# Optimization experiments

Measured on AMD Instinct MI355X. Metric: run time of the kernel, lower is better.

## Reference

```python
import jax, jax.numpy as jnp
import numpy as np

B, T, C, H = 8, 2048, 1024, 128  # batch, seq, embed_dim, head_size

def setup_inputs() -> dict:
    key = jax.random.key(0)
    kx, kk, kq, kv = jax.random.split(key, 4)
    s = 1.0 / np.sqrt(C)  # ~nn.Linear init scale
    return {
        "x": jax.random.normal(kx, (B, T, C), dtype=jnp.float32),
        "Wk": jax.random.normal(kk, (H, C), dtype=jnp.float32) * s,
        "Wq": jax.random.normal(kq, (H, C), dtype=jnp.float32) * s,
        "Wv": jax.random.normal(kv, (H, C), dtype=jnp.float32) * s,
    }

def reference(x, Wk, Wq, Wv):
    b, t, c = x.shape
    # Faithful to source: q uses the KEY projection (bug in original); Wq is unused.
    k = jnp.einsum('btc,hc->bth', x, Wk)   # [B,T,H]
    q = jnp.einsum('btc,hc->bth', x, Wk)   # [B,T,H]  (self.key used for q)
    v = jnp.einsum('btc,hc->bth', x, Wv)   # [B,T,H]
    score = jnp.einsum('bqh,bkh->bqk', q, k) * (c ** -0.5)  # scale by C, per source
    causal = jnp.tril(jnp.ones((t, t), dtype=bool))
    score = jnp.where(causal, score, -jnp.inf)
    attn = jax.nn.softmax(score, axis=-1)   # [B,T,T]
    out = jnp.einsum('bqk,bkh->bqh', attn, v)  # [B,T,H]
    return out
```

## Files before the change

kernel.cpp:

```cpp
#include <hip/hip_runtime.h>
#include <hip/hip_bf16.h>

#define BATCH 8
#define SEQ   2048
#define EMB   1024
#define HD    128

typedef __attribute__((ext_vector_type(8))) short bf16x8;
typedef __attribute__((ext_vector_type(4))) float f32x4;

__device__ __forceinline__ short f2bf(float f) {
    union { float f; unsigned u; } v; v.f = f;
    unsigned r = v.u + 0x7fffu + ((v.u >> 16) & 1u);
    return (short)(r >> 16);
}

__device__ __forceinline__ void glds16(const short* g, short* l) {
    __builtin_amdgcn_global_load_lds(
        (const __attribute__((address_space(1))) unsigned int*)g,
        (__attribute__((address_space(3))) unsigned int*)l, 16, 0, 0);
}


__global__ void prep_w(const float* __restrict__ Wk, const float* __restrict__ Wv,
                       short* __restrict__ Wimg) {
    int g  = blockIdx.x * 256 + threadIdx.x;
    int q  = g & 3;
    int l  = (g >> 2) & 15;
    int f  = (g >> 6) & 7;
    int kk = (g >> 9) & 1;
    int kc = (g >> 10) & 15;
    int nh = (g >> 14) & 1;
    const float* src = (nh ? Wv : Wk) + (size_t)(f * 16 + l) * EMB + kc * 64 + kk * 32 + q * 8;
    float4 f0 = *(const float4*)src;
    float4 f1 = *(const float4*)(src + 4);
    bf16x8 v;
    v[0]=f2bf(f0.x); v[1]=f2bf(f0.y); v[2]=f2bf(f0.z); v[3]=f2bf(f0.w);
    v[4]=f2bf(f1.x); v[5]=f2bf(f1.y); v[6]=f2bf(f1.z); v[7]=f2bf(f1.w);
    *(bf16x8*)&Wimg[(size_t)g * 8] = v;
}

__global__ __launch_bounds__(512, 2)
void proj_kernel(const float* __restrict__ x, const short* __restrict__ Wimg,
                 short* __restrict__ Kimg,
                 short* __restrict__ Vimg)
{
    __shared__ __align__(16) union {
        short A[2][64][72];
        short ep[16384];
    } sm;

    const int tid  = threadIdx.x;
    const int wave = tid >> 6;
    const int lane = tid & 63;
    const int quad = lane >> 4;
    const int l16  = lane & 15;
    const int nh   = wave >> 2;
    const int fb   = (wave & 3) * 2;
    const int mt   = blockIdx.x;
    const int row0 = mt * 64;

    const int srow = tid >> 3, sseg = tid & 7;
    const float* xsrc = x + (size_t)(row0 + srow) * EMB + sseg * 8;
    const short* wsrc = Wimg + (size_t)nh * 131072;

    f32x4 acc[4][2];
#pragma unroll
    for (int a = 0; a < 4; ++a)
#pragma unroll
        for (int c = 0; c < 2; ++c) acc[a][c] = f32x4{0.f, 0.f, 0.f, 0.f};

    {
        float4 a0 = *(const float4*)xsrc;
        float4 a1 = *(const float4*)(xsrc + 4);
        bf16x8 v;
        v[0]=f2bf(a0.x); v[1]=f2bf(a0.y); v[2]=f2bf(a0.z); v[3]=f2bf(a0.w);
        v[4]=f2bf(a1.x); v[5]=f2bf(a1.y); v[6]=f2bf(a1.z); v[7]=f2bf(a1.w);
        *(bf16x8*)&sm.A[0][srow][sseg * 8] = v;
    }
    __syncthreads();

    for (int kc = 0; kc < 16; ++kc) {
        const int cur = kc & 1;
        float4 a0, a1;
        if (kc < 15) {
            const float* nx = xsrc + (kc + 1) * 64;
            a0 = *(const float4*)nx;
            a1 = *(const float4*)(nx + 4);
        }
        const short* wc = wsrc + (size_t)kc * 8192;
        bf16x8 bfr[2][2];
#pragma unroll
        for (int kk = 0; kk < 2; ++kk)
#pragma unroll
            for (int f2 = 0; f2 < 2; ++f2)
                bfr[kk][f2] = *(const bf16x8*)&wc[(((kk * 8 + fb + f2) * 16 + l16) * 4 + quad) * 8];

#pragma unroll
        for (int kk = 0; kk < 2; ++kk)
#pragma unroll
            for (int mf = 0; mf < 4; ++mf) {
                bf16x8 af = *(const bf16x8*)&sm.A[cur][mf * 16 + l16][kk * 32 + quad * 8];
#pragma unroll
                for (int f2 = 0; f2 < 2; ++f2)
                    acc[mf][f2] = __builtin_amdgcn_mfma_f32_16x16x32_bf16(af, bfr[kk][f2], acc[mf][f2], 0, 0, 0);
            }

        if (kc < 15) {
            bf16x8 v;
            v[0]=f2bf(a0.x); v[1]=f2bf(a0.y); v[2]=f2bf(a0.z); v[3]=f2bf(a0.w);
            v[4]=f2bf(a1.x); v[5]=f2bf(a1.y); v[6]=f2bf(a1.z); v[7]=f2bf(a1.w);
            *(bf16x8*)&sm.A[cur ^ 1][srow][sseg * 8] = v;
        }
        __syncthreads();
    }

#pragma unroll
    for (int mf = 0; mf < 4; ++mf)
#pragma unroll
        for (int f2 = 0; f2 < 2; ++f2)
#pragma unroll
            for (int r = 0; r < 4; ++r) {
                const int row = mf * 16 + quad * 4 + r;
                const int h   = (fb + f2) * 16 + l16;
                int idx;
                if (nh == 0)
                    idx = ((((h >> 5) * 4 + (row >> 4)) * 16 + (row & 15)) * 4 + ((h >> 3) & 3)) * 8 + (h & 7);
                else
                    idx = 8192 + ((((row >> 5) * 8 + (h >> 4)) * 16 + (h & 15)) * 4 + ((row >> 3) & 3)) * 8 + (row & 7);
                sm.ep[idx] = f2bf(acc[mf][f2][r]);
            }
    __syncthreads();

    {
#pragma unroll
        for (int i = 0; i < 4; ++i) {
            const int g = i * 512 + tid;
            short* dst = (g < 1024) ? (Kimg + (size_t)mt * 8192 + g * 8)
                                    : (Vimg + (size_t)mt * 8192 + (g - 1024) * 8);
            *(bf16x8*)dst = *(const bf16x8*)&sm.ep[g * 8];
        }
    }
}

#define LOG2E 1.4426950408889634f

__global__ __launch_bounds__(256, 2)
void attn_kernel(const short* __restrict__ Kimg,
                 const short* __restrict__ Vimg,
                 float* __restrict__ out)
{
    __shared__ __align__(16) short kbuf[2][8192];
    __shared__ __align__(16) short vbuf[8192];
    __shared__ __align__(16) short ps[2][1024];
    __shared__ float lsum[4][16];

    const int tid  = threadIdx.x;
    const int wave = tid >> 6;
    const int lane = tid & 63;
    const int quad = lane >> 4;
    const int l16  = lane & 15;

    const int b    = blockIdx.x & 7;
    const int gg   = blockIdx.x >> 3;
    const int G    = (blockIdx.x < 256) ? (63 - gg) : (gg - 32);
    const int qsel = wave >> 1;
    const int p    = wave & 1;
    const int qt   = 2 * G + qsel;
    const int n    = (G >> 1) + 1;

    const short* Kb = Kimg + (size_t)b * 32 * 8192;
    const short* Vb = Vimg + (size_t)b * 32 * 8192;

    bf16x8 qf[4];
    {
        const short* qi = Kb + (size_t)(qt >> 2) * 8192;
        const int jsq = qt & 3;
#pragma unroll
        for (int kc = 0; kc < 4; ++kc)
            qf[kc] = *(const bf16x8*)&qi[(((kc * 4 + jsq) * 16 + l16) * 4 + quad) * 8];
    }

    f32x4 O[4];
#pragma unroll
    for (int f = 0; f < 4; ++f) O[f] = f32x4{0.f, 0.f, 0.f, 0.f};
    float lp[4] = {0.f, 0.f, 0.f, 0.f};

    const float coef = LOG2E * 0.03125f;
    short* psq = ps[qsel];

    {
        const short* sk = Kb + wave * 2048 + lane * 8;
#pragma unroll
        for (int i = 0; i < 4; ++i)
            glds16(sk + i * 512, &kbuf[0][wave * 2048 + i * 512]);
    }

    int cur = 0;
    for (int jt = 0; jt < n; ++jt) {
        asm volatile("s_waitcnt vmcnt(0)" ::: "memory");
        __builtin_amdgcn_s_barrier();

        {
            const short* sv = Vb + (size_t)jt * 8192 + wave * 2048 + lane * 8;
#pragma unroll
            for (int i = 0; i < 4; ++i)
                glds16(sv + i * 512, &vbuf[wave * 2048 + i * 512]);
        }
        const bool more = (jt + 1 < n);
        if (more) {
            const short* sk = Kb + (size_t)(jt + 1) * 8192 + wave * 2048 + lane * 8;
#pragma unroll
            for (int i = 0; i < 4; ++i)
                glds16(sk + i * 512, &kbuf[cur ^ 1][wave * 2048 + i * 512]);
        }

        const short* kt = kbuf[cur];
        f32x4 S[2];
        S[0] = f32x4{0.f, 0.f, 0.f, 0.f};
        S[1] = f32x4{0.f, 0.f, 0.f, 0.f};
#pragma unroll
        for (int kc = 0; kc < 4; ++kc)
#pragma unroll
            for (int j2 = 0; j2 < 2; ++j2) {
                bf16x8 kf = *(const bf16x8*)&kt[((kc * 4 + p * 2 + j2) * 64 + l16 * 4 + quad) * 8];
                S[j2] = __builtin_amdgcn_mfma_f32_16x16x32_bf16(qf[kc], kf, S[j2], 0, 0, 0);
            }

        const bool diag = (jt == n - 1);
#pragma unroll
        for (int j2 = 0; j2 < 2; ++j2) {
            const int js = p * 2 + j2;
            const int jj = jt * 64 + js * 16 + l16;
            const int cb = js * 2 + (l16 >> 3);
            const int e  = l16 & 7;
#pragma unroll
            for (int r = 0; r < 4; ++r) {
                float vv = S[j2][r] * coef;
                if (diag && (jj > qt * 16 + quad * 4 + r)) vv = -INFINITY;
                float pe = exp2f(vv);
                lp[r] += pe;
                const int i8 = quad * 4 + r;
                psq[(i8 * 8 + (cb ^ (i8 & 7))) * 8 + e] = f2bf(pe);
            }
        }

        if (more) asm volatile("s_waitcnt vmcnt(4) lgkmcnt(0)" ::: "memory");
        else      asm volatile("s_waitcnt vmcnt(0) lgkmcnt(0)" ::: "memory");
        __builtin_amdgcn_s_barrier();

#pragma unroll
        for (int jc = 0; jc < 2; ++jc) {
            const int pblk = l16 * 8 + ((jc * 4 + quad) ^ (l16 & 7));
            bf16x8 pa = *(const bf16x8*)&psq[pblk * 8];
#pragma unroll
            for (int fo = 0; fo < 4; ++fo) {
                bf16x8 vf = *(const bf16x8*)&vbuf[((jc * 8 + p * 4 + fo) * 64 + l16 * 4 + quad) * 8];
                O[fo] = __builtin_amdgcn_mfma_f32_16x16x32_bf16(pa, vf, O[fo], 0, 0, 0);
            }
        }
        cur ^= 1;
    }

#pragma unroll
    for (int r = 0; r < 4; ++r) {
        float s = lp[r];
        s += __shfl_xor(s, 1);
        s += __shfl_xor(s, 2);
        s += __shfl_xor(s, 4);
        s += __shfl_xor(s, 8);
        lp[r] = s;
    }
    if (l16 == 0) {
#pragma unroll
        for (int r = 0; r < 4; ++r) lsum[wave][quad * 4 + r] = lp[r];
    }
    __syncthreads();

#pragma unroll
    for (int r = 0; r < 4; ++r) {
        const int row16 = quad * 4 + r;
        const float L   = lsum[qsel * 2][row16] + lsum[qsel * 2 + 1][row16];
        const float inv = 1.f / L;
        const int row   = qt * 16 + row16;
        float* dst = out + (size_t)(b * SEQ + row) * HD + p * 64 + l16;
#pragma unroll
        for (int fo = 0; fo < 4; ++fo)
            dst[fo * 16] = O[fo][r] * inv;
    }
}

extern "C" void kernel_launch(void* const* d_in, const int* in_sizes, int n_in,
                              void* d_out, int out_size, void* d_ws, size_t ws_size,
                              hipStream_t stream) {
    const float* x  = (const float*)d_in[0];
    const float* Wk = (const float*)d_in[1];
    const float* Wv = (const float*)d_in[3];
    float* out = (float*)d_out;

    short* Wimg = (short*)d_ws;
    short* Kimg = Wimg + (size_t)262144;
    short* Vimg = Kimg + (size_t)BATCH * 32 * 8192;

    prep_w<<<128, 256, 0, stream>>>(Wk, Wv, Wimg);
    proj_kernel<<<256, 512, 0, stream>>>(x, Wimg, Kimg, Vimg);
    attn_kernel<<<512, 256, 0, stream>>>(Kimg, Vimg, out);
}
```

Measured before the change: 143.8 us.

## Halve projection row tile to 32 rows and prefetch weights two-deep

```diff
diff --git a/kernel.cpp b/kernel.cpp
--- a/kernel.cpp
+++ b/kernel.cpp
@@ -40,14 +40,14 @@
     *(bf16x8*)&Wimg[(size_t)g * 8] = v;
 }
 
-__global__ __launch_bounds__(512, 2)
+__global__ __launch_bounds__(256, 2)
 void proj_kernel(const float* __restrict__ x, const short* __restrict__ Wimg,
                  short* __restrict__ Kimg,
                  short* __restrict__ Vimg)
 {
     __shared__ __align__(16) union {
-        short A[2][64][72];
-        short ep[16384];
+        short A[2][32][72];
+        short ep[8192];
     } sm;
 
     const int tid  = threadIdx.x;
@@ -55,21 +55,25 @@
     const int lane = tid & 63;
     const int quad = lane >> 4;
     const int l16  = lane & 15;
-    const int nh   = wave >> 2;
-    const int fb   = (wave & 3) * 2;
+    const int nh   = wave >> 1;
+    const int fb   = (wave & 1) * 4;
     const int mt   = blockIdx.x;
-    const int row0 = mt * 64;
+    const int half = mt & 1;
+    const int t64  = mt >> 1;
+    const int row0 = mt * 32;
 
     const int srow = tid >> 3, sseg = tid & 7;
     const float* xsrc = x + (size_t)(row0 + srow) * EMB + sseg * 8;
     const short* wsrc = Wimg + (size_t)nh * 131072;
 
-    f32x4 acc[4][2];
-#pragma unroll
-    for (int a = 0; a < 4; ++a)
-#pragma unroll
-        for (int c = 0; c < 2; ++c) acc[a][c] = f32x4{0.f, 0.f, 0.f, 0.f};
-
+    f32x4 acc[2][4];
+#pragma unroll
+    for (int a = 0; a < 2; ++a)
+#pragma unroll
+        for (int c = 0; c < 4; ++c) acc[a][c] = f32x4{0.f, 0.f, 0.f, 0.f};
+
+    float4 p0, p1;
+    bf16x8 bw[2][4];
     {
         float4 a0 = *(const float4*)xsrc;
         float4 a1 = *(const float4*)(xsrc + 4);
@@ -77,68 +81,96 @@
         v[0]=f2bf(a0.x); v[1]=f2bf(a0.y); v[2]=f2bf(a0.z); v[3]=f2bf(a0.w);
         v[4]=f2bf(a1.x); v[5]=f2bf(a1.y); v[6]=f2bf(a1.z); v[7]=f2bf(a1.w);
         *(bf16x8*)&sm.A[0][srow][sseg * 8] = v;
+        p0 = *(const float4*)(xsrc + 64);
+        p1 = *(const float4*)(xsrc + 68);
+#pragma unroll
+        for (int kk = 0; kk < 2; ++kk)
+#pragma unroll
+            for (int fi = 0; fi < 4; ++fi)
+                bw[kk][fi] = *(const bf16x8*)&wsrc[(((kk * 8 + fb + fi) * 16 + l16) * 4 + quad) * 8];
     }
     __syncthreads();
 
+#pragma unroll 2
     for (int kc = 0; kc < 16; ++kc) {
         const int cur = kc & 1;
-        float4 a0, a1;
+        float4 n0, n1;
+        if (kc < 14) {
+            const float* nx = xsrc + (kc + 2) * 64;
+            n0 = *(const float4*)nx;
+            n1 = *(const float4*)(nx + 4);
+        }
+        bf16x8 nw[2][4];
         if (kc < 15) {
-            const float* nx = xsrc + (kc + 1) * 64;
-            a0 = *(const float4*)nx;
-            a1 = *(const float4*)(nx + 4);
-        }
-        const short* wc = wsrc + (size_t)kc * 8192;
-        bf16x8 bfr[2][2];
+            const short* wc = wsrc + (size_t)(kc + 1) * 8192;
+#pragma unroll
+            for (int kk = 0; kk < 2; ++kk)
+#pragma unroll
+                for (int fi = 0; fi < 4; ++fi)
+                    nw[kk][fi] = *(const bf16x8*)&wc[(((kk * 8 + fb + fi) * 16 + l16) * 4 + quad) * 8];
+        }
+
 #pragma unroll
         for (int kk = 0; kk < 2; ++kk)
 #pragma unroll
-            for (int f2 = 0; f2 < 2; ++f2)
-                bfr[kk][f2] = *(const bf16x8*)&wc[(((kk * 8 + fb + f2) * 16 + l16) * 4 + quad) * 8];
-
-#pragma unroll
-        for (int kk = 0; kk < 2; ++kk)
-#pragma unroll
-            for (int mf = 0; mf < 4; ++mf) {
+            for (int mf = 0; mf < 2; ++mf) {
                 bf16x8 af = *(const bf16x8*)&sm.A[cur][mf * 16 + l16][kk * 32 + quad * 8];
 #pragma unroll
-                for (int f2 = 0; f2 < 2; ++f2)
-                    acc[mf][f2] = __builtin_amdgcn_mfma_f32_16x16x32_bf16(af, bfr[kk][f2], acc[mf][f2], 0, 0, 0);
+                for (int fi = 0; fi < 4; ++fi)
+                    acc[mf][fi] = __builtin_amdgcn_mfma_f32_16x16x32_bf16(af, bw[kk][fi], acc[mf][fi], 0, 0, 0);
             }
 
         if (kc < 15) {
             bf16x8 v;
-            v[0]=f2bf(a0.x); v[1]=f2bf(a0.y); v[2]=f2bf(a0.z); v[3]=f2bf(a0.w);
-            v[4]=f2bf(a1.x); v[5]=f2bf(a1.y); v[6]=f2bf(a1.z); v[7]=f2bf(a1.w);
+            v[0]=f2bf(p0.x); v[1]=f2bf(p0.y); v[2]=f2bf(p0.z); v[3]=f2bf(p0.w);
+            v[4]=f2bf(p1.x); v[5]=f2bf(p1.y); v[6]=f2bf(p1.z); v[7]=f2bf(p1.w);
             *(bf16x8*)&sm.A[cur ^ 1][srow][sseg * 8] = v;
         }
+        if (kc < 14) { p0 = n0; p1 = n1; }
+        if (kc < 15) {
+#pragma unroll
+            for (int kk = 0; kk < 2; ++kk)
+#pragma unroll
+                for (int fi = 0; fi < 4; ++fi) bw[kk][fi] = nw[kk][fi];
+        }
         __syncthreads();
     }
 
 #pragma unroll
-    for (int mf = 0; mf < 4; ++mf)
-#pragma unroll
-        for (int f2 = 0; f2 < 2; ++f2)
+    for (int mf = 0; mf < 2; ++mf)
+#pragma unroll
+        for (int fi = 0; fi < 4; ++fi)
 #pragma unroll
             for (int r = 0; r < 4; ++r) {
-                const int row = mf * 16 + quad * 4 + r;
-                const int h   = (fb + f2) * 16 + l16;
+                const int rl = mf * 16 + quad * 4 + r;
+                const int h  = (fb + fi) * 16 + l16;
                 int idx;
                 if (nh == 0)
-                    idx = ((((h >> 5) * 4 + (row >> 4)) * 16 + (row & 15)) * 4 + ((h >> 3) & 3)) * 8 + (h & 7);
+                    idx = ((((h >> 5) * 2 + ((rl >> 4) & 1)) * 16 + (rl & 15)) * 4 + ((h >> 3) & 3)) * 8 + (h & 7);
                 else
-                    idx = 8192 + ((((row >> 5) * 8 + (h >> 4)) * 16 + (h & 15)) * 4 + ((row >> 3) & 3)) * 8 + (row & 7);
-                sm.ep[idx] = f2bf(acc[mf][f2][r]);
+                    idx = 4096 + (((h >> 4) * 16 + (h & 15)) * 4 + ((rl >> 3) & 3)) * 8 + (rl & 7);
+                sm.ep[idx] = f2bf(acc[mf][fi][r]);
             }
     __syncthreads();
 
     {
 #pragma unroll
         for (int i = 0; i < 4; ++i) {
-            const int g = i * 512 + tid;
-            short* dst = (g < 1024) ? (Kimg + (size_t)mt * 8192 + g * 8)
-                                    : (Vimg + (size_t)mt * 8192 + (g - 1024) * 8);
-            *(bf16x8*)dst = *(const bf16x8*)&sm.ep[g * 8];
+            const int g = i * 256 + tid;
+            short* dst;
+            const short* src;
+            if (g < 512) {
+                const int u = g;
+                const int gofs = ((((u >> 7) * 4 + half * 2 + ((u >> 6) & 1)) * 16
+                                   + ((u >> 2) & 15)) * 4 + (u & 3)) * 8;
+                dst = Kimg + (size_t)t64 * 8192 + gofs;
+                src = &sm.ep[u * 8];
+            } else {
+                const int u = g - 512;
+                dst = Vimg + (size_t)t64 * 8192 + half * 4096 + u * 8;
+                src = &sm.ep[4096 + u * 8];
+            }
+            *(bf16x8*)dst = *(const bf16x8*)src;
         }
     }
 }
@@ -303,6 +335,6 @@
     short* Vimg = Kimg + (size_t)BATCH * 32 * 8192;
 
     prep_w<<<128, 256, 0, stream>>>(Wk, Wv, Wimg);
-    proj_kernel<<<256, 512, 0, stream>>>(x, Wimg, Kimg, Vimg);
+    proj_kernel<<<512, 256, 0, stream>>>(x, Wimg, Kimg, Vimg);
     attn_kernel<<<512, 256, 0, stream>>>(Kimg, Vimg, out);
 }
```

Result: slower. 148.9 us (+3.6%).

## Repartition attention waves so each handles both query tiles over its key slice

Applied to the files above, without the earlier changes.

```diff
diff --git a/kernel.cpp b/kernel.cpp
--- a/kernel.cpp
+++ b/kernel.cpp
@@ -153,10 +153,10 @@
     __shared__ __align__(16) short kbuf[2][8192];
     __shared__ __align__(16) short vbuf[8192];
     __shared__ __align__(16) short ps[2][1024];
-    __shared__ float lsum[4][16];
+    __shared__ float lsum[4][2][16];
 
     const int tid  = threadIdx.x;
-    const int wave = tid >> 6;
+    const int w    = tid >> 6;
     const int lane = tid & 63;
     const int quad = lane >> 4;
     const int l16  = lane & 15;
@@ -164,36 +164,37 @@
     const int b    = blockIdx.x & 7;
     const int gg   = blockIdx.x >> 3;
     const int G    = (blockIdx.x < 256) ? (63 - gg) : (gg - 32);
-    const int qsel = wave >> 1;
-    const int p    = wave & 1;
-    const int qt   = 2 * G + qsel;
     const int n    = (G >> 1) + 1;
 
     const short* Kb = Kimg + (size_t)b * 32 * 8192;
     const short* Vb = Vimg + (size_t)b * 32 * 8192;
 
-    bf16x8 qf[4];
+    bf16x8 qf[2][4];
     {
-        const short* qi = Kb + (size_t)(qt >> 2) * 8192;
-        const int jsq = qt & 3;
-#pragma unroll
-        for (int kc = 0; kc < 4; ++kc)
-            qf[kc] = *(const bf16x8*)&qi[(((kc * 4 + jsq) * 16 + l16) * 4 + quad) * 8];
-    }
-
-    f32x4 O[4];
-#pragma unroll
-    for (int f = 0; f < 4; ++f) O[f] = f32x4{0.f, 0.f, 0.f, 0.f};
-    float lp[4] = {0.f, 0.f, 0.f, 0.f};
+        const short* qi = Kb + (size_t)(G >> 1) * 8192;
+#pragma unroll
+        for (int qsel = 0; qsel < 2; ++qsel) {
+            const int jsq = (2 * G + qsel) & 3;
+#pragma unroll
+            for (int kc = 0; kc < 4; ++kc)
+                qf[qsel][kc] = *(const bf16x8*)&qi[(((kc * 4 + jsq) * 16 + l16) * 4 + quad) * 8];
+        }
+    }
+
+    f32x4 O[2][2];
+#pragma unroll
+    for (int a = 0; a < 2; ++a)
+#pragma unroll
+        for (int c = 0; c < 2; ++c) O[a][c] = f32x4{0.f, 0.f, 0.f, 0.f};
+    float lp[2][4] = {{0.f,0.f,0.f,0.f},{0.f,0.f,0.f,0.f}};
 
     const float coef = LOG2E * 0.03125f;
-    short* psq = ps[qsel];
 
     {
-        const short* sk = Kb + wave * 2048 + lane * 8;
+        const short* sk = Kb + w * 2048 + lane * 8;
 #pragma unroll
         for (int i = 0; i < 4; ++i)
-            glds16(sk + i * 512, &kbuf[0][wave * 2048 + i * 512]);
+            glds16(sk + i * 512, &kbuf[0][w * 2048 + i * 512]);
     }
 
     int cur = 0;
@@ -202,44 +203,48 @@
         __builtin_amdgcn_s_barrier();
 
         {
-            const short* sv = Vb + (size_t)jt * 8192 + wave * 2048 + lane * 8;
+            const short* sv = Vb + (size_t)jt * 8192 + w * 2048 + lane * 8;
 #pragma unroll
             for (int i = 0; i < 4; ++i)
-                glds16(sv + i * 512, &vbuf[wave * 2048 + i * 512]);
+                glds16(sv + i * 512, &vbuf[w * 2048 + i * 512]);
         }
         const bool more = (jt + 1 < n);
         if (more) {
-            const short* sk = Kb + (size_t)(jt + 1) * 8192 + wave * 2048 + lane * 8;
+            const short* sk = Kb + (size_t)(jt + 1) * 8192 + w * 2048 + lane * 8;
 #pragma unroll
             for (int i = 0; i < 4; ++i)
-                glds16(sk + i * 512, &kbuf[cur ^ 1][wave * 2048 + i * 512]);
+                glds16(sk + i * 512, &kbuf[cur ^ 1][w * 2048 + i * 512]);
         }
 
         const short* kt = kbuf[cur];
+        bf16x8 kf[4];
+#pragma unroll
+        for (int kc = 0; kc < 4; ++kc)
+            kf[kc] = *(const bf16x8*)&kt[((kc * 4 + w) * 64 + l16 * 4 + quad) * 8];
+
         f32x4 S[2];
         S[0] = f32x4{0.f, 0.f, 0.f, 0.f};
         S[1] = f32x4{0.f, 0.f, 0.f, 0.f};
 #pragma unroll
         for (int kc = 0; kc < 4; ++kc)
 #pragma unroll
-            for (int j2 = 0; j2 < 2; ++j2) {
-                bf16x8 kf = *(const bf16x8*)&kt[((kc * 4 + p * 2 + j2) * 64 + l16 * 4 + quad) * 8];
-                S[j2] = __builtin_amdgcn_mfma_f32_16x16x32_bf16(qf[kc], kf, S[j2], 0, 0, 0);
-            }
+            for (int qsel = 0; qsel < 2; ++qsel)
+                S[qsel] = __builtin_amdgcn_mfma_f32_16x16x32_bf16(qf[qsel][kc], kf[kc], S[qsel], 0, 0, 0);
 
         const bool diag = (jt == n - 1);
-#pragma unroll
-        for (int j2 = 0; j2 < 2; ++j2) {
-            const int js = p * 2 + j2;
-            const int jj = jt * 64 + js * 16 + l16;
-            const int cb = js * 2 + (l16 >> 3);
-            const int e  = l16 & 7;
+        const int jj = jt * 64 + w * 16 + l16;
+        const int cb = w * 2 + (l16 >> 3);
+        const int e  = l16 & 7;
+#pragma unroll
+        for (int qsel = 0; qsel < 2; ++qsel) {
+            const int qtq = 2 * G + qsel;
+            short* psq = ps[qsel];
 #pragma unroll
             for (int r = 0; r < 4; ++r) {
-                float vv = S[j2][r] * coef;
-                if (diag && (jj > qt * 16 + quad * 4 + r)) vv = -INFINITY;
+                float vv = S[qsel][r] * coef;
+                if (diag && (jj > qtq * 16 + quad * 4 + r)) vv = -INFINITY;
                 float pe = exp2f(vv);
-                lp[r] += pe;
+                lp[qsel][r] += pe;
                 const int i8 = quad * 4 + r;
                 psq[(i8 * 8 + (cb ^ (i8 & 7))) * 8 + e] = f2bf(pe);
             }
@@ -251,42 +256,52 @@
 
 #pragma unroll
         for (int jc = 0; jc < 2; ++jc) {
-            const int pblk = l16 * 8 + ((jc * 4 + quad) ^ (l16 & 7));
-            bf16x8 pa = *(const bf16x8*)&psq[pblk * 8];
-#pragma unroll
-            for (int fo = 0; fo < 4; ++fo) {
-                bf16x8 vf = *(const bf16x8*)&vbuf[((jc * 8 + p * 4 + fo) * 64 + l16 * 4 + quad) * 8];
-                O[fo] = __builtin_amdgcn_mfma_f32_16x16x32_bf16(pa, vf, O[fo], 0, 0, 0);
+            bf16x8 vf0 = *(const bf16x8*)&vbuf[((jc * 8 + w * 2 + 0) * 64 + l16 * 4 + quad) * 8];
+            bf16x8 vf1 = *(const bf16x8*)&vbuf[((jc * 8 + w * 2 + 1) * 64 + l16 * 4 + quad) * 8];
+#pragma unroll
+            for (int qsel = 0; qsel < 2; ++qsel) {
+                const int pblk = l16 * 8 + ((jc * 4 + quad) ^ (l16 & 7));
+                bf16x8 pa = *(const bf16x8*)&ps[qsel][pblk * 8];
+                O[qsel][0] = __builtin_amdgcn_mfma_f32_16x16x32_bf16(pa, vf0, O[qsel][0], 0, 0, 0);
+                O[qsel][1] = __builtin_amdgcn_mfma_f32_16x16x32_bf16(pa, vf1, O[qsel][1], 0, 0, 0);
             }
         }
         cur ^= 1;
     }
 
 #pragma unroll
-    for (int r = 0; r < 4; ++r) {
-        float s = lp[r];
-        s += __shfl_xor(s, 1);
-        s += __shfl_xor(s, 2);
-        s += __shfl_xor(s, 4);
-        s += __shfl_xor(s, 8);
-        lp[r] = s;
-    }
+    for (int qsel = 0; qsel < 2; ++qsel)
+#pragma unroll
+        for (int r = 0; r < 4; ++r) {
+            float s = lp[qsel][r];
+            s += __shfl_xor(s, 1);
+            s += __shfl_xor(s, 2);
+            s += __shfl_xor(s, 4);
+            s += __shfl_xor(s, 8);
+            lp[qsel][r] = s;
+        }
     if (l16 == 0) {
 #pragma unroll
-        for (int r = 0; r < 4; ++r) lsum[wave][quad * 4 + r] = lp[r];
+        for (int qsel = 0; qsel < 2; ++qsel)
+#pragma unroll
+            for (int r = 0; r < 4; ++r) lsum[w][qsel][quad * 4 + r] = lp[qsel][r];
     }
     __syncthreads();
 
 #pragma unroll
-    for (int r = 0; r < 4; ++r) {
-        const int row16 = quad * 4 + r;
-        const float L   = lsum[qsel * 2][row16] + lsum[qsel * 2 + 1][row16];
-        const float inv = 1.f / L;
-        const int row   = qt * 16 + row16;
-        float* dst = out + (size_t)(b * SEQ + row) * HD + p * 64 + l16;
-#pragma unroll
-        for (int fo = 0; fo < 4; ++fo)
-            dst[fo * 16] = O[fo][r] * inv;
+    for (int qsel = 0; qsel < 2; ++qsel) {
+        const int qtq = 2 * G + qsel;
+#pragma unroll
+        for (int r = 0; r < 4; ++r) {
+            const int row16 = quad * 4 + r;
+            const float L = lsum[0][qsel][row16] + lsum[1][qsel][row16]
+                          + lsum[2][qsel][row16] + lsum[3][qsel][row16];
+            const float inv = 1.f / L;
+            const int row   = qtq * 16 + row16;
+            float* dst = out + (size_t)(b * SEQ + row) * HD + w * 32 + l16;
+            dst[0]  = O[qsel][0][r] * inv;
+            dst[16] = O[qsel][1][r] * inv;
+        }
     }
 }
 
```

New measurement: 149.2 us. +3.8%, slower.

## Deepen projection GEMM prefetch pipeline and use lightweight LDS-only barriers

Applied to the files above, without the earlier changes.

```diff
diff --git a/kernel.cpp b/kernel.cpp
--- a/kernel.cpp
+++ b/kernel.cpp
@@ -70,6 +70,9 @@
 #pragma unroll
         for (int c = 0; c < 2; ++c) acc[a][c] = f32x4{0.f, 0.f, 0.f, 0.f};
 
+    float4 pxA0, pxA1, pxB0, pxB1;
+    bf16x8 bwA[2][2], bwB[2][2];
+
     {
         float4 a0 = *(const float4*)xsrc;
         float4 a1 = *(const float4*)(xsrc + 4);
@@ -77,43 +80,59 @@
         v[0]=f2bf(a0.x); v[1]=f2bf(a0.y); v[2]=f2bf(a0.z); v[3]=f2bf(a0.w);
         v[4]=f2bf(a1.x); v[5]=f2bf(a1.y); v[6]=f2bf(a1.z); v[7]=f2bf(a1.w);
         *(bf16x8*)&sm.A[0][srow][sseg * 8] = v;
-    }
-    __syncthreads();
-
-    for (int kc = 0; kc < 16; ++kc) {
-        const int cur = kc & 1;
-        float4 a0, a1;
-        if (kc < 15) {
-            const float* nx = xsrc + (kc + 1) * 64;
-            a0 = *(const float4*)nx;
-            a1 = *(const float4*)(nx + 4);
-        }
-        const short* wc = wsrc + (size_t)kc * 8192;
-        bf16x8 bfr[2][2];
+        pxB0 = *(const float4*)(xsrc + 64);
+        pxB1 = *(const float4*)(xsrc + 68);
 #pragma unroll
         for (int kk = 0; kk < 2; ++kk)
 #pragma unroll
             for (int f2 = 0; f2 < 2; ++f2)
-                bfr[kk][f2] = *(const bf16x8*)&wc[(((kk * 8 + fb + f2) * 16 + l16) * 4 + quad) * 8];
-
-#pragma unroll
-        for (int kk = 0; kk < 2; ++kk)
-#pragma unroll
-            for (int mf = 0; mf < 4; ++mf) {
-                bf16x8 af = *(const bf16x8*)&sm.A[cur][mf * 16 + l16][kk * 32 + quad * 8];
-#pragma unroll
-                for (int f2 = 0; f2 < 2; ++f2)
-                    acc[mf][f2] = __builtin_amdgcn_mfma_f32_16x16x32_bf16(af, bfr[kk][f2], acc[mf][f2], 0, 0, 0);
-            }
-
-        if (kc < 15) {
-            bf16x8 v;
-            v[0]=f2bf(a0.x); v[1]=f2bf(a0.y); v[2]=f2bf(a0.z); v[3]=f2bf(a0.w);
-            v[4]=f2bf(a1.x); v[5]=f2bf(a1.y); v[6]=f2bf(a1.z); v[7]=f2bf(a1.w);
-            *(bf16x8*)&sm.A[cur ^ 1][srow][sseg * 8] = v;
-        }
-        __syncthreads();
-    }
+                bwA[kk][f2] = *(const bf16x8*)&wsrc[(((kk * 8 + fb + f2) * 16 + l16) * 4 + quad) * 8];
+    }
+    asm volatile("s_waitcnt lgkmcnt(0)" ::: "memory");
+    __builtin_amdgcn_s_barrier();
+
+#define PROJ_STEP(KC, BWC, BWN, PXN0, PXN1, PXS0, PXS1, CL, NL, DOX, DOW, DOST) \
+    {                                                                           \
+        if (DOX) {                                                              \
+            const float* nx_ = xsrc + ((KC) + 2) * 64;                          \
+            PXN0 = *(const float4*)nx_;                                         \
+            PXN1 = *(const float4*)(nx_ + 4);                                   \
+        }                                                                       \
+        if (DOW) {                                                              \
+            const short* wn_ = wsrc + (size_t)((KC) + 1) * 8192;                \
+            _Pragma("unroll")                                                   \
+            for (int kk = 0; kk < 2; ++kk)                                      \
+                _Pragma("unroll")                                               \
+                for (int f2 = 0; f2 < 2; ++f2)                                  \
+                    BWN[kk][f2] = *(const bf16x8*)&wn_[(((kk * 8 + fb + f2) * 16 + l16) * 4 + quad) * 8]; \
+        }                                                                       \
+        _Pragma("unroll")                                                       \
+        for (int kk = 0; kk < 2; ++kk)                                          \
+            _Pragma("unroll")                                                   \
+            for (int mf = 0; mf < 4; ++mf) {                                    \
+                bf16x8 af_ = *(const bf16x8*)&sm.A[CL][mf * 16 + l16][kk * 32 + quad * 8]; \
+                _Pragma("unroll")                                               \
+                for (int f2 = 0; f2 < 2; ++f2)                                  \
+                    acc[mf][f2] = __builtin_amdgcn_mfma_f32_16x16x32_bf16(af_, BWC[kk][f2], acc[mf][f2], 0, 0, 0); \
+            }                                                                   \
+        if (DOST) {                                                             \
+            bf16x8 v_;                                                          \
+            v_[0]=f2bf(PXS0.x); v_[1]=f2bf(PXS0.y); v_[2]=f2bf(PXS0.z); v_[3]=f2bf(PXS0.w); \
+            v_[4]=f2bf(PXS1.x); v_[5]=f2bf(PXS1.y); v_[6]=f2bf(PXS1.z); v_[7]=f2bf(PXS1.w); \
+            *(bf16x8*)&sm.A[NL][srow][sseg * 8] = v_;                           \
+        }                                                                       \
+        asm volatile("s_waitcnt lgkmcnt(0)" ::: "memory");                      \
+        __builtin_amdgcn_s_barrier();                                           \
+    }
+
+    for (int kp = 0; kp < 7; ++kp) {
+        const int kc = kp * 2;
+        PROJ_STEP(kc,     bwA, bwB, pxA0, pxA1, pxB0, pxB1, 0, 1, 1, 1, 1)
+        PROJ_STEP(kc + 1, bwB, bwA, pxB0, pxB1, pxA0, pxA1, 1, 0, 1, 1, 1)
+    }
+    PROJ_STEP(14, bwA, bwB, pxA0, pxA1, pxB0, pxB1, 0, 1, 0, 1, 1)
+    PROJ_STEP(15, bwB, bwA, pxB0, pxB1, pxA0, pxA1, 1, 0, 0, 0, 0)
+#undef PROJ_STEP
 
 #pragma unroll
     for (int mf = 0; mf < 4; ++mf)
```

Result: no change. 142.8 us (median of 2 runs) (-0.7%).
